# Performance work log

Measured on AMD Instinct MI355X. Metric: run time of the kernel, lower is better.

Reference implementation:

```python
import jax, jax.numpy as jnp
import numpy as np

NUM_HEADS = 16
DIM = 1024


def setup_inputs() -> dict:
    key = jax.random.key(0)
    kx, kw, kb = jax.random.split(key, 3)
    x = jax.random.normal(kx, (4, 2048, DIM), dtype=jnp.float32)
    # torch Linear(dim, 3*dim): weight [3d, d], bias [3d]; store as [d, 3d] for x @ W
    W_qkv = jax.random.normal(kw, (DIM, 3 * DIM), dtype=jnp.float32) * (1.0 / np.sqrt(DIM))
    b_qkv = jax.random.normal(kb, (3 * DIM,), dtype=jnp.float32) * 0.01
    return {"x": x, "W_qkv": W_qkv, "b_qkv": b_qkv}


def reference(x, W_qkv, b_qkv):
    b, t, d = x.shape
    h = NUM_HEADS
    hd = d // h
    qkv = x @ W_qkv + b_qkv  # [b, t, 3d]
    q, k, v = jnp.split(qkv, 3, axis=-1)
    # [b, t, h, hd] -> [b, h, t, hd]
    q = q.reshape(b, t, h, hd).transpose(0, 2, 1, 3)
    k = k.reshape(b, t, h, hd).transpose(0, 2, 1, 3)
    v = v.reshape(b, t, h, hd).transpose(0, 2, 1, 3)
    # NOTE: original scales by sqrt(full dim d), not head_dim
    logits = jnp.einsum("bhqc,bhkc->bhqk", q, k) / jnp.sqrt(jnp.float32(d))
    causal = jnp.tril(jnp.ones((t, t), dtype=bool))  # [t, t]
    logits = jnp.where(causal, logits, -jnp.inf)
    attn = jax.nn.softmax(logits, axis=-1)
    out = jnp.einsum("bhqk,bhkc->bhqc", attn, v)  # [b, h, t, hd]
    return out.transpose(0, 2, 1, 3).reshape(b, t, d)
```

## Files before the change

### kernel.cpp

```cpp
#include <hip/hip_runtime.h>
#include <hip/hip_bf16.h>

#define D_MODEL 1024
#define N3      3072
#define TSEQ    2048
#define M_TOT   8192

typedef __bf16 bf16_8 __attribute__((ext_vector_type(8)));
typedef float  f32x4  __attribute__((ext_vector_type(4)));
typedef short  s16x4  __attribute__((ext_vector_type(4)));

static __device__ __forceinline__ unsigned short f2bf(float f) {
  __hip_bfloat16 h = __float2bfloat16(f);
  unsigned short u;
  __builtin_memcpy(&u, &h, 2);
  return u;
}
static __device__ __forceinline__ unsigned pack2(float lo, float hi) {
  return (unsigned)f2bf(lo) | ((unsigned)f2bf(hi) << 16);
}
static __device__ __forceinline__ void gload16(const void* g, void* l) {
  __builtin_amdgcn_global_load_lds((const __attribute__((address_space(1))) void*)g,
                                   (__attribute__((address_space(3))) void*)l, 16, 0, 0);
}

__global__ void cvt_x_kernel(const float* __restrict__ x, __bf16* __restrict__ xb) {
  size_t i = (size_t)blockIdx.x * 256 + threadIdx.x;
  float4 v = *(const float4*)(x + i * 4);
  ushort4 o;
  o.x = f2bf(v.x); o.y = f2bf(v.y); o.z = f2bf(v.z); o.w = f2bf(v.w);
  *(ushort4*)((unsigned short*)xb + i * 4) = o;
}

__global__ void cvt_w_kernel(const float* __restrict__ W, __bf16* __restrict__ WT) {
  __shared__ unsigned short tl[64][68];
  int t = threadIdx.x;
  int n0 = blockIdx.x * 64, k0 = blockIdx.y * 64;
  int rr = t >> 4, cc = (t & 15) * 4;
#pragma unroll
  for (int i = 0; i < 4; ++i) {
    int r = rr + i * 16;
    float4 v = *(const float4*)(W + (size_t)(k0 + r) * N3 + n0 + cc);
    tl[r][cc] = f2bf(v.x); tl[r][cc + 1] = f2bf(v.y);
    tl[r][cc + 2] = f2bf(v.z); tl[r][cc + 3] = f2bf(v.w);
  }
  __syncthreads();
#pragma unroll
  for (int i = 0; i < 4; ++i) {
    int rc = rr + i * 16;
    ushort4 o;
    o.x = tl[cc + 0][rc]; o.y = tl[cc + 1][rc];
    o.z = tl[cc + 2][rc]; o.w = tl[cc + 3][rc];
    *(ushort4*)((unsigned short*)WT + (size_t)(n0 + rc) * D_MODEL + k0 + cc) = o;
  }
}

__global__ void vtrans_kernel(const __bf16* __restrict__ qkv, __bf16* __restrict__ VT) {
  __shared__ unsigned short tl[64][68];
  int t = threadIdx.x;
  int t0 = blockIdx.x * 64;
  int bh = blockIdx.y;
  int b = bh >> 4, h = bh & 15;
  int rr = t >> 4, cc = (t & 15) * 4;
  const unsigned short* q16 = (const unsigned short*)qkv;
#pragma unroll
  for (int i = 0; i < 4; ++i) {
    int r = rr + i * 16;
    ushort4 v = *(const ushort4*)(q16 + (size_t)(b * TSEQ + t0 + r) * N3 + 2048 + h * 64 + cc);
    tl[r][cc] = v.x; tl[r][cc + 1] = v.y; tl[r][cc + 2] = v.z; tl[r][cc + 3] = v.w;
  }
  __syncthreads();
#pragma unroll
  for (int i = 0; i < 4; ++i) {
    int rc = rr + i * 16;
    ushort4 o;
    o.x = tl[cc + 0][rc]; o.y = tl[cc + 1][rc];
    o.z = tl[cc + 2][rc]; o.w = tl[cc + 3][rc];
    *(ushort4*)((unsigned short*)VT + (size_t)(bh * 64 + rc) * TSEQ + t0 + cc) = o;
  }
}

__global__ __launch_bounds__(256, 2) void gemm_qkv_kernel(
    const __bf16* __restrict__ A, const __bf16* __restrict__ Bt,
    const float* __restrict__ bias, __bf16* __restrict__ C) {
  __shared__ __align__(16) __bf16 Al[2][4096];
  __shared__ __align__(16) __bf16 Bl[2][4096];
  int tid = threadIdx.x;
  int wave = tid >> 6, lane = tid & 63;
  int lr = lane & 15, lg = lane >> 4;
  int m0 = blockIdx.x * 128, n0 = blockIdx.y * 128;
  int wm = (wave >> 1) * 64, wn = (wave & 1) * 64;

  const f32x4 fz = {0.f, 0.f, 0.f, 0.f};
  f32x4 acc[4][4];
#pragma unroll
  for (int i = 0; i < 4; ++i)
#pragma unroll
    for (int j = 0; j < 4; ++j) acc[i][j] = fz;

  auto stage = [&](int buf, int kt) {
#pragma unroll
    for (int call = 0; call < 2; ++call) {
      int cb = call * 256 + wave * 64;
      int c = cb + lane;
      int row = c >> 2;
      int cir = (c & 3) ^ ((row >> 1) & 3);
      gload16(A + (size_t)(m0 + row) * D_MODEL + kt * 32 + cir * 8, &Al[buf][cb * 8]);
      gload16(Bt + (size_t)(n0 + row) * D_MODEL + kt * 32 + cir * 8, &Bl[buf][cb * 8]);
    }
  };

  stage(0, 0);
  __syncthreads();
  for (int kt = 0; kt < 32; ++kt) {
    int buf = kt & 1;
    if (kt + 1 < 32) stage(buf ^ 1, kt + 1);
    bf16_8 af[4], bv[4];
#pragma unroll
    for (int mb = 0; mb < 4; ++mb) {
      int row = wm + mb * 16 + lr;
      int cir = lg ^ ((row >> 1) & 3);
      af[mb] = *(const bf16_8*)&Al[buf][row * 32 + cir * 8];
    }
#pragma unroll
    for (int nb = 0; nb < 4; ++nb) {
      int row = wn + nb * 16 + lr;
      int cir = lg ^ ((row >> 1) & 3);
      bv[nb] = *(const bf16_8*)&Bl[buf][row * 32 + cir * 8];
    }
#pragma unroll
    for (int mb = 0; mb < 4; ++mb)
#pragma unroll
      for (int nb = 0; nb < 4; ++nb)
        acc[mb][nb] = __builtin_amdgcn_mfma_f32_16x16x32_bf16(af[mb], bv[nb], acc[mb][nb], 0, 0, 0);
    __syncthreads();
  }

  const float SC = 0.04508422f;
  float oscale = (n0 < 1024) ? SC : 1.0f;
  float bvs[4];
#pragma unroll
  for (int nb = 0; nb < 4; ++nb) bvs[nb] = bias[n0 + wn + nb * 16 + lr];
  unsigned short* C16 = (unsigned short*)C;
#pragma unroll
  for (int mb = 0; mb < 4; ++mb)
#pragma unroll
    for (int nb = 0; nb < 4; ++nb)
#pragma unroll
      for (int r = 0; r < 4; ++r) {
        int row = m0 + wm + mb * 16 + lg * 4 + r;
        int col = n0 + wn + nb * 16 + lr;
        C16[(size_t)row * N3 + col] = f2bf((acc[mb][nb][r] + bvs[nb]) * oscale);
      }
}

__global__ __launch_bounds__(256, 4) void attn_kernel(
    const __bf16* __restrict__ qkv, const __bf16* __restrict__ VT,
    float* __restrict__ out) {
  __shared__ __align__(16) char smem[16384];
  __bf16* Kl = (__bf16*)smem;
  __bf16* Vl = (__bf16*)(smem + 8192);

  int lin = blockIdx.x;
  int y = lin & 63;
  int qt = 31 - (lin >> 6);
  int bh = (y & 7) * 8 + (y >> 3);
  int b = bh >> 4, h = bh & 15;
  int tid = threadIdx.x, wave = tid >> 6, lane = tid & 63;
  int lr = lane & 15, lg = lane >> 4;
  int q0 = qt * 64 + wave * 16;

  const __bf16* Kg = qkv + (size_t)b * TSEQ * N3 + 1024 + h * 64;
  const __bf16* Vg = VT + (size_t)bh * 64 * TSEQ;

  auto stage = [&](int kv0) {
#pragma unroll
    for (int call = 0; call < 2; ++call) {
      int cb = call * 256 + wave * 64;
      int c = cb + lane;
      int row = c >> 3;
      int cir = (c & 7) ^ (row & 7);
      gload16(Kg + (size_t)(kv0 + row) * N3 + cir * 8, Kl + cb * 8);
      gload16(Vg + (size_t)row * TSEQ + kv0 + cir * 8, Vl + cb * 8);
    }
  };

  bf16_8 qf[2];
#pragma unroll
  for (int kk = 0; kk < 2; ++kk)
    qf[kk] = *(const bf16_8*)&qkv[(size_t)(b * TSEQ + q0 + lr) * N3 + h * 64 + kk * 32 + lg * 8];

  float ps_acc = 0.f;
  const f32x4 fz = {0.f, 0.f, 0.f, 0.f};
  f32x4 oacc[4];
#pragma unroll
  for (int i = 0; i < 4; ++i) oacc[i] = fz;

  int ntiles = qt + 1;
  stage(0);
  __syncthreads();
  for (int tt = 0; tt < ntiles; ++tt) {
    int kv0 = tt * 64;
    {
      f32x4 st[4];
#pragma unroll
      for (int i = 0; i < 4; ++i) st[i] = fz;
#pragma unroll
      for (int kk = 0; kk < 2; ++kk) {
        bf16_8 kf[4];
#pragma unroll
        for (int mb = 0; mb < 4; ++mb) {
          int row = mb * 16 + lr;
          int cir = (kk * 4 + lg) ^ (row & 7);
          kf[mb] = *(const bf16_8*)&Kl[row * 64 + cir * 8];
        }
        __builtin_amdgcn_s_setprio(1);
#pragma unroll
        for (int mb = 0; mb < 4; ++mb)
          st[mb] = __builtin_amdgcn_mfma_f32_16x16x32_bf16(kf[mb], qf[kk], st[mb], 0, 0, 0);
        __builtin_amdgcn_s_setprio(0);
      }
      unsigned pw[4][2];
      if (kv0 + 63 > q0) {
#pragma unroll
        for (int mb = 0; mb < 4; ++mb) {
          float p[4];
#pragma unroll
          for (int r = 0; r < 4; ++r) {
            int kv = kv0 + mb * 16 + lg * 4 + r;
            float s = (kv > q0 + lr) ? -1e30f : st[mb][r];
            p[r] = __builtin_amdgcn_exp2f(s);
            ps_acc += p[r];
          }
          pw[mb][0] = pack2(p[0], p[1]);
          pw[mb][1] = pack2(p[2], p[3]);
        }
      } else {
#pragma unroll
        for (int mb = 0; mb < 4; ++mb) {
          float p[4];
#pragma unroll
          for (int r = 0; r < 4; ++r) {
            p[r] = __builtin_amdgcn_exp2f(st[mb][r]);
            ps_acc += p[r];
          }
          pw[mb][0] = pack2(p[0], p[1]);
          pw[mb][1] = pack2(p[2], p[3]);
        }
      }
#pragma unroll
      for (int mb = 0; mb < 4; ++mb) {
        s16x4 vf[4];
        int chunk = mb * 2 + (lg >> 1);
#pragma unroll
        for (int mbc = 0; mbc < 4; ++mbc) {
          int row = mbc * 16 + lr;
          int cir = chunk ^ (row & 7);
          vf[mbc] = *(const s16x4*)((const char*)Vl + row * 128 + cir * 16 + (lg & 1) * 8);
        }
        union { unsigned u[2]; s16x4 v; } pf;
        pf.u[0] = pw[mb][0];
        pf.u[1] = pw[mb][1];
        __builtin_amdgcn_s_setprio(1);
#pragma unroll
        for (int mbc = 0; mbc < 4; ++mbc)
          oacc[mbc] = __builtin_amdgcn_mfma_f32_16x16x16bf16_1k(vf[mbc], pf.v, oacc[mbc], 0, 0, 0);
        __builtin_amdgcn_s_setprio(0);
      }
    }
    __syncthreads();
    if (tt + 1 < ntiles) {
      stage((tt + 1) * 64);
      __syncthreads();
    }
  }

  ps_acc += __shfl_xor(ps_acc, 16, 64);
  ps_acc += __shfl_xor(ps_acc, 32, 64);
  float invl = 1.f / ps_acc;
  float* dst = out + (size_t)(b * TSEQ + q0 + lr) * D_MODEL + h * 64 + lg * 4;
#pragma unroll
  for (int mbc = 0; mbc < 4; ++mbc) {
    float4 v;
    v.x = oacc[mbc][0] * invl; v.y = oacc[mbc][1] * invl;
    v.z = oacc[mbc][2] * invl; v.w = oacc[mbc][3] * invl;
    *(float4*)(dst + mbc * 16) = v;
  }
}

extern "C" void kernel_launch(void* const* d_in, const int* in_sizes, int n_in,
                              void* d_out, int out_size, void* d_ws, size_t ws_size,
                              hipStream_t stream) {
  const float* x = (const float*)d_in[0];
  const float* W = (const float*)d_in[1];
  const float* bias = (const float*)d_in[2];
  float* out = (float*)d_out;
  char* ws = (char*)d_ws;
  __bf16* xb  = (__bf16*)(ws);
  __bf16* WT  = (__bf16*)(ws + (size_t)16777216);
  __bf16* qkv = (__bf16*)(ws + (size_t)23068672);
  __bf16* VT  = (__bf16*)(ws + (size_t)73400320);

  hipLaunchKernelGGL(cvt_x_kernel, dim3(8192), dim3(256), 0, stream, x, xb);
  hipLaunchKernelGGL(cvt_w_kernel, dim3(48, 16), dim3(256), 0, stream, W, WT);
  hipLaunchKernelGGL(gemm_qkv_kernel, dim3(64, 24), dim3(256), 0, stream, xb, WT, bias, qkv);
  hipLaunchKernelGGL(vtrans_kernel, dim3(32, 64), dim3(256), 0, stream, qkv, VT);
  hipLaunchKernelGGL(attn_kernel, dim3(2048), dim3(256), 0, stream, qkv, VT, out);
}
```

Before: 144.6 us.

## Deepen LDS pipelining in QKV GEMM and attention with single-barrier loops

Result: slower. 151.2 us (+4.6%).

```diff
diff --git a/kernel.cpp b/kernel.cpp
--- a/kernel.cpp
+++ b/kernel.cpp
@@ -83,8 +83,8 @@
 __global__ __launch_bounds__(256, 2) void gemm_qkv_kernel(
     const __bf16* __restrict__ A, const __bf16* __restrict__ Bt,
     const float* __restrict__ bias, __bf16* __restrict__ C) {
-  __shared__ __align__(16) __bf16 Al[2][4096];
-  __shared__ __align__(16) __bf16 Bl[2][4096];
+  __shared__ __align__(16) __bf16 Al[4][4096];
+  __shared__ __align__(16) __bf16 Bl[4][4096];
   int tid = threadIdx.x;
   int wave = tid >> 6, lane = tid & 63;
   int lr = lane & 15, lg = lane >> 4;
@@ -110,11 +110,24 @@
     }
   };
 
-  stage(0, 0);
-  __syncthreads();
+  stage(0, 0); stage(1, 1);
+  asm volatile("s_waitcnt vmcnt(4)" ::: "memory");
+  __builtin_amdgcn_sched_barrier(0);
+  __builtin_amdgcn_s_barrier();
+
   for (int kt = 0; kt < 32; ++kt) {
-    int buf = kt & 1;
-    if (kt + 1 < 32) stage(buf ^ 1, kt + 1);
+    if (kt + 2 < 32) {
+      stage((kt + 2) & 3, kt + 2);
+      asm volatile("s_waitcnt vmcnt(8)" ::: "memory");
+    } else if (kt + 1 < 32) {
+      asm volatile("s_waitcnt vmcnt(4)" ::: "memory");
+    } else {
+      asm volatile("s_waitcnt vmcnt(0)" ::: "memory");
+    }
+    __builtin_amdgcn_sched_barrier(0);
+    __builtin_amdgcn_s_barrier();
+
+    int buf = kt & 3;
     bf16_8 af[4], bv[4];
 #pragma unroll
     for (int mb = 0; mb < 4; ++mb) {
@@ -128,12 +141,13 @@
       int cir = lg ^ ((row >> 1) & 3);
       bv[nb] = *(const bf16_8*)&Bl[buf][row * 32 + cir * 8];
     }
+    __builtin_amdgcn_s_setprio(1);
 #pragma unroll
     for (int mb = 0; mb < 4; ++mb)
 #pragma unroll
       for (int nb = 0; nb < 4; ++nb)
         acc[mb][nb] = __builtin_amdgcn_mfma_f32_16x16x32_bf16(af[mb], bv[nb], acc[mb][nb], 0, 0, 0);
-    __syncthreads();
+    __builtin_amdgcn_s_setprio(0);
   }
 
   const float SC = 0.04508422f;
@@ -157,9 +171,7 @@
 __global__ __launch_bounds__(256, 4) void attn_kernel(
     const __bf16* __restrict__ qkv, const __bf16* __restrict__ VT,
     float* __restrict__ out) {
-  __shared__ __align__(16) char smem[16384];
-  __bf16* Kl = (__bf16*)smem;
-  __bf16* Vl = (__bf16*)(smem + 8192);
+  __shared__ __align__(16) char smem[49152];
 
   int lin = blockIdx.x;
   int y = lin & 63;
@@ -173,7 +185,9 @@
   const __bf16* Kg = qkv + (size_t)b * TSEQ * N3 + 1024 + h * 64;
   const __bf16* Vg = VT + (size_t)bh * 64 * TSEQ;
 
-  auto stage = [&](int kv0) {
+  auto stage = [&](int buf, int kv0) {
+    __bf16* Kl = (__bf16*)(smem + buf * 16384);
+    __bf16* Vl = (__bf16*)(smem + buf * 16384 + 8192);
 #pragma unroll
     for (int call = 0; call < 2; ++call) {
       int cb = call * 256 + wave * 64;
@@ -197,82 +211,88 @@
   for (int i = 0; i < 4; ++i) oacc[i] = fz;
 
   int ntiles = qt + 1;
-  stage(0);
-  __syncthreads();
+  stage(0, 0);
+  int cur = 0;
   for (int tt = 0; tt < ntiles; ++tt) {
+    int nxt = (cur == 2) ? 0 : cur + 1;
+    if (tt + 1 < ntiles) {
+      stage(nxt, (tt + 1) * 64);
+      asm volatile("s_waitcnt vmcnt(4)" ::: "memory");
+    } else {
+      asm volatile("s_waitcnt vmcnt(0)" ::: "memory");
+    }
+    __builtin_amdgcn_sched_barrier(0);
+    __builtin_amdgcn_s_barrier();
+
+    const __bf16* Kb = (const __bf16*)(smem + cur * 16384);
+    const __bf16* Vb = (const __bf16*)(smem + cur * 16384 + 8192);
     int kv0 = tt * 64;
-    {
-      f32x4 st[4];
-#pragma unroll
-      for (int i = 0; i < 4; ++i) st[i] = fz;
-#pragma unroll
-      for (int kk = 0; kk < 2; ++kk) {
-        bf16_8 kf[4];
-#pragma unroll
-        for (int mb = 0; mb < 4; ++mb) {
-          int row = mb * 16 + lr;
-          int cir = (kk * 4 + lg) ^ (row & 7);
-          kf[mb] = *(const bf16_8*)&Kl[row * 64 + cir * 8];
+    f32x4 st[4];
+#pragma unroll
+    for (int i = 0; i < 4; ++i) st[i] = fz;
+#pragma unroll
+    for (int kk = 0; kk < 2; ++kk) {
+      bf16_8 kf[4];
+#pragma unroll
+      for (int mb = 0; mb < 4; ++mb) {
+        int row = mb * 16 + lr;
+        int cir = (kk * 4 + lg) ^ (row & 7);
+        kf[mb] = *(const bf16_8*)&Kb[row * 64 + cir * 8];
+      }
+      __builtin_amdgcn_s_setprio(1);
+#pragma unroll
+      for (int mb = 0; mb < 4; ++mb)
+        st[mb] = __builtin_amdgcn_mfma_f32_16x16x32_bf16(kf[mb], qf[kk], st[mb], 0, 0, 0);
+      __builtin_amdgcn_s_setprio(0);
+    }
+    unsigned pw[4][2];
+    if (kv0 + 63 > q0) {
+#pragma unroll
+      for (int mb = 0; mb < 4; ++mb) {
+        float p[4];
+#pragma unroll
+        for (int r = 0; r < 4; ++r) {
+          int kv = kv0 + mb * 16 + lg * 4 + r;
+          float s = (kv > q0 + lr) ? -1e30f : st[mb][r];
+          p[r] = __builtin_amdgcn_exp2f(s);
+          ps_acc += p[r];
         }
-        __builtin_amdgcn_s_setprio(1);
-#pragma unroll
-        for (int mb = 0; mb < 4; ++mb)
-          st[mb] = __builtin_amdgcn_mfma_f32_16x16x32_bf16(kf[mb], qf[kk], st[mb], 0, 0, 0);
-        __builtin_amdgcn_s_setprio(0);
-      }
-      unsigned pw[4][2];
-      if (kv0 + 63 > q0) {
-#pragma unroll
-        for (int mb = 0; mb < 4; ++mb) {
-          float p[4];
-#pragma unroll
-          for (int r = 0; r < 4; ++r) {
-            int kv = kv0 + mb * 16 + lg * 4 + r;
-            float s = (kv > q0 + lr) ? -1e30f : st[mb][r];
-            p[r] = __builtin_amdgcn_exp2f(s);
-            ps_acc += p[r];
-          }
-          pw[mb][0] = pack2(p[0], p[1]);
-          pw[mb][1] = pack2(p[2], p[3]);
+        pw[mb][0] = pack2(p[0], p[1]);
+        pw[mb][1] = pack2(p[2], p[3]);
+      }
+    } else {
+#pragma unroll
+      for (int mb = 0; mb < 4; ++mb) {
+        float p[4];
+#pragma unroll
+        for (int r = 0; r < 4; ++r) {
+          p[r] = __builtin_amdgcn_exp2f(st[mb][r]);
+          ps_acc += p[r];
         }
-      } else {
-#pragma unroll
-        for (int mb = 0; mb < 4; ++mb) {
-          float p[4];
-#pragma unroll
-          for (int r = 0; r < 4; ++r) {
-            p[r] = __builtin_amdgcn_exp2f(st[mb][r]);
-            ps_acc += p[r];
-          }
-          pw[mb][0] = pack2(p[0], p[1]);
-          pw[mb][1] = pack2(p[2], p[3]);
-        }
-      }
-#pragma unroll
-      for (int mb = 0; mb < 4; ++mb) {
-        s16x4 vf[4];
-        int chunk = mb * 2 + (lg >> 1);
-#pragma unroll
-        for (int mbc = 0; mbc < 4; ++mbc) {
-          int row = mbc * 16 + lr;
-          int cir = chunk ^ (row & 7);
-          vf[mbc] = *(const s16x4*)((const char*)Vl + row * 128 + cir * 16 + (lg & 1) * 8);
-        }
-        union { unsigned u[2]; s16x4 v; } pf;
-        pf.u[0] = pw[mb][0];
-        pf.u[1] = pw[mb][1];
-        __builtin_amdgcn_s_setprio(1);
-#pragma unroll
-        for (int mbc = 0; mbc < 4; ++mbc)
-          oacc[mbc] = __builtin_amdgcn_mfma_f32_16x16x16bf16_1k(vf[mbc], pf.v, oacc[mbc], 0, 0, 0);
-        __builtin_amdgcn_s_setprio(0);
-      }
-    }
-    __syncthreads();
-    if (tt + 1 < ntiles) {
-      stage((tt + 1) * 64);
-      __syncthreads();
-    }
+        pw[mb][0] = pack2(p[0], p[1]);
+        pw[mb][1] = pack2(p[2], p[3]);
+      }
+    }
+#pragma unroll
+    for (int mb = 0; mb < 4; ++mb) {
+      s16x4 vf[4];
+      int chunk = mb * 2 + (lg >> 1);
+#pragma unroll
+      for (int mbc = 0; mbc < 4; ++mbc) {
+        int row = mbc * 16 + lr;
+        int cir = chunk ^ (row & 7);
+        vf[mbc] = *(const s16x4*)((const char*)Vb + row * 128 + cir * 16 + (lg & 1) * 8);
+      }
+      union { unsigned u[2]; s16x4 v; } pf;
+      pf.u[0] = pw[mb][0];
+      pf.u[1] = pw[mb][1];
+      __builtin_amdgcn_s_setprio(1);
+#pragma unroll
+      for (int mbc = 0; mbc < 4; ++mbc)
+        oacc[mbc] = __builtin_amdgcn_mfma_f32_16x16x16bf16_1k(vf[mbc], pf.v, oacc[mbc], 0, 0, 0);
+      __builtin_amdgcn_s_setprio(0);
+    }
+    cur = nxt;
   }
 
   ps_acc += __shfl_xor(ps_acc, 16, 64);
```
